# Kernel optimization log

Hardware: AMD Instinct MI355X
Metric: run time of the kernel (lower is better)

## Reference

```python
import jax, jax.numpy as jnp
import numpy as np

BATCH, N_STEPS, STATE_DIM = 8192, 128, 16
HIDDEN = 50
IN0 = STATE_DIM + 1  # features + prev_delta


def _lstm_cell(x, h, c, w_ih, w_hh, b):
    # PyTorch gate order: i, f, g, o
    gates = x @ w_ih.T + h @ w_hh.T + b  # (B, 4H)
    i, f, g, o = jnp.split(gates, 4, axis=-1)
    c_new = jax.nn.sigmoid(f) * c + jax.nn.sigmoid(i) * jnp.tanh(g)
    h_new = jax.nn.sigmoid(o) * jnp.tanh(c_new)
    return h_new, c_new


def setup_inputs() -> dict:
    key = jax.random.key(0)
    ks = jax.random.split(key, 8)
    s = 0.1
    return {
        "features": jax.random.normal(ks[0], (BATCH, N_STEPS, STATE_DIM), dtype=jnp.float32),
        "w_ih0": jax.random.normal(ks[1], (4 * HIDDEN, IN0), dtype=jnp.float32) * s,
        "w_hh0": jax.random.normal(ks[2], (4 * HIDDEN, HIDDEN), dtype=jnp.float32) * s,
        "b_0": jnp.zeros((4 * HIDDEN,), dtype=jnp.float32),  # bias_ih + bias_hh (both init to 0)
        "w_ih1": jax.random.normal(ks[3], (4 * HIDDEN, HIDDEN), dtype=jnp.float32) * s,
        "w_hh1": jax.random.normal(ks[4], (4 * HIDDEN, HIDDEN), dtype=jnp.float32) * s,
        "b_1": jnp.zeros((4 * HIDDEN,), dtype=jnp.float32),
        "w_fc1": jax.random.normal(ks[5], (HIDDEN // 2, HIDDEN), dtype=jnp.float32) * s,
        "b_fc1": jnp.zeros((HIDDEN // 2,), dtype=jnp.float32),
        "w_fc2": jax.random.normal(ks[6], (1, HIDDEN // 2), dtype=jnp.float32) * s,
        "b_fc2": jnp.zeros((1,), dtype=jnp.float32),
    }


def reference(features, w_ih0, w_hh0, b_0, w_ih1, w_hh1, b_1, w_fc1, b_fc1, w_fc2, b_fc2):
    B = features.shape[0]
    feats_t = jnp.swapaxes(features, 0, 1)  # (T, B, state_dim)
    z = jnp.zeros((B, HIDDEN), dtype=features.dtype)
    init = (z, z, z, z, jnp.zeros((B, 1), dtype=features.dtype))

    def step(carry, x_t):
        h0, c0, h1, c1, prev_delta = carry
        x = jnp.concatenate([x_t, prev_delta], axis=-1)  # (B, state_dim+1)
        h0, c0 = _lstm_cell(x, h0, c0, w_ih0, w_hh0, b_0)
        h1, c1 = _lstm_cell(h0, h1, c1, w_ih1, w_hh1, b_1)
        delta = jax.nn.relu(h1 @ w_fc1.T + b_fc1) @ w_fc2.T + b_fc2  # (B, 1)
        return (h0, c0, h1, c1, delta), delta[:, 0]

    _, deltas = jax.lax.scan(step, init, feats_t)  # (T, B)
    return jnp.swapaxes(deltas, 0, 1)  # (B, T)
```

## Files before the change

kernel.cpp:

```cpp
#include <hip/hip_runtime.h>
#include <math.h>

#define BATCH    8192
#define TSTEPS   128
#define SDIM     16
#define HID      50
#define IN0      17
#define BT       16
#define NTHREADS 512

#define RS      168
#define OFF_H0  32
#define OFF_H1  96
#define W0K     96
#define W1K     128
#define WFK     64

typedef _Float16 half_t;
typedef __attribute__((ext_vector_type(8))) _Float16 half8;
typedef __attribute__((ext_vector_type(4))) float    floatx4;

#define MFMA16(a, b, c) __builtin_amdgcn_mfma_f32_16x16x32_f16((a), (b), (c), 0, 0, 0)

__device__ __forceinline__ float sig_u(float x) {
    float e = __expf(-x);
    return __builtin_amdgcn_rcpf(1.0f + e);
}
__device__ __forceinline__ float tanh_u(float x) {
    float e = __expf(-2.0f * x);
    return fmaf(2.0f, __builtin_amdgcn_rcpf(1.0f + e), -1.0f);
}
__device__ __forceinline__ void hsplit(float v, half_t* hp, half_t* lp) {
    half_t h = (half_t)v;
    *hp = h;
    *lp = (half_t)(v - (float)h);
}

__global__ __launch_bounds__(NTHREADS, 4)
void lstm2_w8_kernel(const float* __restrict__ feat,
                     const float* __restrict__ w_ih0,
                     const float* __restrict__ w_hh0,
                     const float* __restrict__ b_0,
                     const float* __restrict__ w_ih1,
                     const float* __restrict__ w_hh1,
                     const float* __restrict__ b_1,
                     const float* __restrict__ w_fc1,
                     const float* __restrict__ b_fc1,
                     const float* __restrict__ w_fc2,
                     const float* __restrict__ b_fc2,
                     float* __restrict__ out)
{
    __shared__ __align__(16) half_t smW[64 * W1K];
    __shared__ __align__(16) half_t Xh[2][BT * RS];
    __shared__ __align__(16) half_t Xl[2][BT * RS];

    const int tid  = threadIdx.x;
    const int lane = tid & 63;
    const int wv   = tid >> 6;
    const int quad = lane >> 4;
    const int col  = lane & 15;
    const int k0q  = quad * 8;
    const int b0   = blockIdx.x * BT;
    const int tcnt = (wv < 6) ? 2 : (wv == 6 ? 1 : 0);

    auto w0val = [&](int r, int k) -> float {
        if (r >= 200) return 0.0f;
        int j = r >> 2, q = r & 3, orig = q * HID + j;
        if (k < IN0)  return w_ih0[orig * IN0 + k];
        if (k == IN0) return b_0[orig];
        if (k < OFF_H0) return 0.0f;
        int u = k - OFF_H0;
        return (u < HID) ? w_hh0[orig * HID + u] : 0.0f;
    };
    auto w1val = [&](int r, int k) -> float {
        if (r >= 200) return 0.0f;
        int j = r >> 2, q = r & 3, orig = q * HID + j;
        if (k < 64) {
            if (k < HID)  return w_ih1[orig * HID + k];
            if (k == HID) return b_1[orig];
            return 0.0f;
        }
        int u = k - 64;
        return (u < HID) ? w_hh1[orig * HID + u] : 0.0f;
    };

    half8 a0f[3][2], a1f[4][2];
    const int lbase = 32 * (wv & 1) + col;
    #pragma unroll 1
    for (int c = 0; c < 4; ++c) {
        for (int i = tid; i < 64 * W0K; i += NTHREADS) {
            int r = i / W0K, k = i - r * W0K;
            smW[i] = (half_t)w0val(64 * c + r, k);
        }
        __syncthreads();
        if ((wv >> 1) == c) {
            #pragma unroll
            for (int kt = 0; kt < 3; ++kt)
                #pragma unroll
                for (int ti = 0; ti < 2; ++ti)
                    a0f[kt][ti] = *(const half8*)(smW + (lbase + 16 * ti) * W0K + 32 * kt + k0q);
        }
        __syncthreads();
    }
    #pragma unroll 1
    for (int c = 0; c < 4; ++c) {
        for (int i = tid; i < 64 * W1K; i += NTHREADS) {
            int r = i >> 7, k = i & 127;
            smW[i] = (half_t)w1val(64 * c + r, k);
        }
        __syncthreads();
        if ((wv >> 1) == c) {
            #pragma unroll
            for (int kt = 0; kt < 4; ++kt)
                #pragma unroll
                for (int ti = 0; ti < 2; ++ti)
                    a1f[kt][ti] = *(const half8*)(smW + (lbase + 16 * ti) * W1K + 32 * kt + k0q);
        }
        __syncthreads();
    }
    for (int i = tid; i < 32 * WFK; i += NTHREADS) {
        int r = i >> 6, k = i & 63;
        float v = 0.0f;
        if (r < 25) { if (k < HID) v = w_fc1[r * HID + k]; else if (k == HID) v = b_fc1[r]; }
        smW[i] = (half_t)v;
    }
    __syncthreads();
    half8 wff[2][2];
    #pragma unroll
    for (int kt = 0; kt < 2; ++kt)
        #pragma unroll
        for (int tf = 0; tf < 2; ++tf)
            wff[kt][tf] = *(const half8*)(smW + (16 * tf + col) * WFK + 32 * kt + k0q);

    for (int i = tid; i < BT * RS; i += NTHREADS) {
        Xh[0][i] = (half_t)0.0f; Xl[0][i] = (half_t)0.0f;
        Xh[1][i] = (half_t)0.0f; Xl[1][i] = (half_t)0.0f;
    }
    __syncthreads();
    if (tid < BT) {
        Xh[0][tid * RS + OFF_H0 + HID] = (half_t)1.0f;
        Xh[1][tid * RS + OFF_H0 + HID] = (half_t)1.0f;
        Xh[0][tid * RS + OFF_H1 + HID] = (half_t)1.0f;
        Xh[1][tid * RS + OFF_H1 + HID] = (half_t)1.0f;
    }
    const bool stager = (tid < BT * SDIM);
    const int  xs = tid >> 4, xk = tid & 15;
    const size_t fbase = (size_t)(b0 + (stager ? xs : 0)) * (TSTEPS * SDIM) + xk;
    if (stager) hsplit(feat[fbase], &Xh[0][xs * RS + xk], &Xl[0][xs * RS + xk]);

    floatx4 w2r[2];
    { floatx4 z = {0.f, 0.f, 0.f, 0.f}; w2r[0] = z; w2r[1] = z; }
    #pragma unroll
    for (int tf = 0; tf < 2; ++tf)
        #pragma unroll
        for (int r5 = 0; r5 < 4; ++r5) {
            int r = 16 * tf + 4 * quad + r5;
            if (r < 25) w2r[tf][r5] = w_fc2[r];
        }
    const float bf2 = b_fc2[0];

    const half8   hz = {0, 0, 0, 0, 0, 0, 0, 0};
    const floatx4 fz = {0.f, 0.f, 0.f, 0.f};
    float c0s[2] = {0.f, 0.f};
    float c1s[2] = {0.f, 0.f};
    half_t dh = (half_t)0.0f, dl = (half_t)0.0f;

    half_t* Xhc = Xh[0]; half_t* Xlc = Xl[0];
    half_t* Xhn = Xh[1]; half_t* Xln = Xl[1];
    __syncthreads();

    for (int t = 0; t < TSTEPS; ++t) {
        float fnext = 0.0f;
        if (stager && (t + 1 < TSTEPS)) fnext = feat[fbase + (size_t)(t + 1) * SDIM];

        floatx4 acc[2]; acc[0] = fz; acc[1] = fz;
        if (tcnt > 0) {
            half8 bh0, bl0;
            if (quad < 2) {
                bh0 = *(const half8*)(Xhc + col * RS + k0q);
                bl0 = *(const half8*)(Xlc + col * RS + k0q);
            } else {
                bh0 = hz; bl0 = hz;
                if (quad == 2) { bh0[0] = dh; bh0[1] = (half_t)1.0f; bl0[0] = dl; }
            }
            #pragma unroll
            for (int ti = 0; ti < 2; ++ti)
                if (ti < tcnt) {
                    acc[ti] = MFMA16(a0f[0][ti], bh0, acc[ti]);
                    acc[ti] = MFMA16(a0f[0][ti], bl0, acc[ti]);
                }
            #pragma unroll
            for (int kt = 1; kt < 3; ++kt) {
                half8 bh = *(const half8*)(Xhc + col * RS + OFF_H0 + 32 * (kt - 1) + k0q);
                half8 bl = *(const half8*)(Xlc + col * RS + OFF_H0 + 32 * (kt - 1) + k0q);
                #pragma unroll
                for (int ti = 0; ti < 2; ++ti)
                    if (ti < tcnt) {
                        acc[ti] = MFMA16(a0f[kt][ti], bh, acc[ti]);
                        acc[ti] = MFMA16(a0f[kt][ti], bl, acc[ti]);
                    }
            }
        }

        #pragma unroll
        for (int ti = 0; ti < 2; ++ti)
            if (ti < tcnt) {
                int u = 8 * wv + 4 * ti + quad;
                float i_ = sig_u(acc[ti][0]);
                float f_ = sig_u(acc[ti][1]);
                float g_ = tanh_u(acc[ti][2]);
                float o_ = sig_u(acc[ti][3]);
                float c  = f_ * c0s[ti] + i_ * g_;
                c0s[ti]  = c;
                float hv = o_ * tanh_u(c);
                if (u < HID) {
                    half_t hh, hl; hsplit(hv, &hh, &hl);
                    Xhn[col * RS + OFF_H0 + u] = hh;
                    Xln[col * RS + OFF_H0 + u] = hl;
                }
            }
        __syncthreads();

        if (stager && (t + 1 < TSTEPS))
            hsplit(fnext, &Xhn[xs * RS + xk], &Xln[xs * RS + xk]);

        floatx4 acc1[2]; acc1[0] = fz; acc1[1] = fz;
        if (tcnt > 0) {
            #pragma unroll
            for (int kt = 0; kt < 2; ++kt) {
                half8 bh = *(const half8*)(Xhn + col * RS + OFF_H0 + 32 * kt + k0q);
                half8 bl = *(const half8*)(Xln + col * RS + OFF_H0 + 32 * kt + k0q);
                #pragma unroll
                for (int ti = 0; ti < 2; ++ti)
                    if (ti < tcnt) {
                        acc1[ti] = MFMA16(a1f[kt][ti], bh, acc1[ti]);
                        acc1[ti] = MFMA16(a1f[kt][ti], bl, acc1[ti]);
                    }
            }
            #pragma unroll
            for (int kt = 2; kt < 4; ++kt) {
                half8 bh = *(const half8*)(Xhc + col * RS + OFF_H1 + 32 * (kt - 2) + k0q);
                half8 bl = *(const half8*)(Xlc + col * RS + OFF_H1 + 32 * (kt - 2) + k0q);
                #pragma unroll
                for (int ti = 0; ti < 2; ++ti)
                    if (ti < tcnt) {
                        acc1[ti] = MFMA16(a1f[kt][ti], bh, acc1[ti]);
                        acc1[ti] = MFMA16(a1f[kt][ti], bl, acc1[ti]);
                    }
            }
        }

        #pragma unroll
        for (int ti = 0; ti < 2; ++ti)
            if (ti < tcnt) {
                int u = 8 * wv + 4 * ti + quad;
                float i_ = sig_u(acc1[ti][0]);
                float f_ = sig_u(acc1[ti][1]);
                float g_ = tanh_u(acc1[ti][2]);
                float o_ = sig_u(acc1[ti][3]);
                float c  = f_ * c1s[ti] + i_ * g_;
                c1s[ti]  = c;
                float hv = o_ * tanh_u(c);
                if (u < HID) {
                    half_t hh, hl; hsplit(hv, &hh, &hl);
                    Xhn[col * RS + OFF_H1 + u] = hh;
                    Xln[col * RS + OFF_H1 + u] = hl;
                }
            }
        __syncthreads();

        floatx4 accf[2]; accf[0] = fz; accf[1] = fz;
        #pragma unroll
        for (int kt = 0; kt < 2; ++kt) {
            half8 bh = *(const half8*)(Xhn + col * RS + OFF_H1 + 32 * kt + k0q);
            half8 bl = *(const half8*)(Xln + col * RS + OFF_H1 + 32 * kt + k0q);
            #pragma unroll
            for (int tf = 0; tf < 2; ++tf) {
                accf[tf] = MFMA16(wff[kt][tf], bh, accf[tf]);
                accf[tf] = MFMA16(wff[kt][tf], bl, accf[tf]);
            }
        }
        float p = 0.0f;
        #pragma unroll
        for (int tf = 0; tf < 2; ++tf)
            #pragma unroll
            for (int r5 = 0; r5 < 4; ++r5)
                p += w2r[tf][r5] * fmaxf(accf[tf][r5], 0.0f);
        p += __shfl_xor(p, 16);
        p += __shfl_xor(p, 32);
        float d = p + bf2;
        if (wv == 0 && lane < 16)
            out[(size_t)(b0 + lane) * TSTEPS + t] = d;
        hsplit(d, &dh, &dl);

        half_t* tp;
        tp = Xhc; Xhc = Xhn; Xhn = tp;
        tp = Xlc; Xlc = Xln; Xln = tp;
    }
}

extern "C" void kernel_launch(void* const* d_in, const int* in_sizes, int n_in,
                              void* d_out, int out_size, void* d_ws, size_t ws_size,
                              hipStream_t stream) {
    const float* feat  = (const float*)d_in[0];
    const float* w_ih0 = (const float*)d_in[1];
    const float* w_hh0 = (const float*)d_in[2];
    const float* b_0   = (const float*)d_in[3];
    const float* w_ih1 = (const float*)d_in[4];
    const float* w_hh1 = (const float*)d_in[5];
    const float* b_1   = (const float*)d_in[6];
    const float* w_fc1 = (const float*)d_in[7];
    const float* b_fc1 = (const float*)d_in[8];
    const float* w_fc2 = (const float*)d_in[9];
    const float* b_fc2 = (const float*)d_in[10];
    float* out = (float*)d_out;

    dim3 grid(BATCH / BT);
    dim3 block(NTHREADS);
    hipLaunchKernelGGL(lstm2_w8_kernel, grid, block, 0, stream,
                       feat, w_ih0, w_hh0, b_0, w_ih1, w_hh1, b_1,
                       w_fc1, b_fc1, w_fc2, b_fc2, out);
}
```

Measured before the change: 473.3 us.

## Fold biases into accumulators, apply prev-delta in fp32, split hi/lo MFMA chains

Biases move out of the weight matrices and become the initial MFMA accumulator values, and the prev_delta input column is applied as an fp32 FMA after the matmul. This removes the bias/one columns from shared memory and drops the idle 8th wave (448 threads). The hi and lo MFMA products now go to separate accumulators, which breaks the serial dependency chain so two chains can interleave, at the cost of extra registers and a vector add per gate.

```diff
diff --git a/kernel.cpp b/kernel.cpp
--- a/kernel.cpp
+++ b/kernel.cpp
@@ -7,7 +7,7 @@
 #define HID      50
 #define IN0      17
 #define BT       16
-#define NTHREADS 512
+#define NTHREADS 448
 
 #define RS      168
 #define OFF_H0  32
@@ -61,13 +61,11 @@
     const int col  = lane & 15;
     const int k0q  = quad * 8;
     const int b0   = blockIdx.x * BT;
-    const int tcnt = (wv < 6) ? 2 : (wv == 6 ? 1 : 0);
 
     auto w0val = [&](int r, int k) -> float {
         if (r >= 200) return 0.0f;
         int j = r >> 2, q = r & 3, orig = q * HID + j;
-        if (k < IN0)  return w_ih0[orig * IN0 + k];
-        if (k == IN0) return b_0[orig];
+        if (k < SDIM)   return w_ih0[orig * IN0 + k];
         if (k < OFF_H0) return 0.0f;
         int u = k - OFF_H0;
         return (u < HID) ? w_hh0[orig * HID + u] : 0.0f;
@@ -75,11 +73,7 @@
     auto w1val = [&](int r, int k) -> float {
         if (r >= 200) return 0.0f;
         int j = r >> 2, q = r & 3, orig = q * HID + j;
-        if (k < 64) {
-            if (k < HID)  return w_ih1[orig * HID + k];
-            if (k == HID) return b_1[orig];
-            return 0.0f;
-        }
+        if (k < 64) return (k < HID) ? w_ih1[orig * HID + k] : 0.0f;
         int u = k - 64;
         return (u < HID) ? w_hh1[orig * HID + u] : 0.0f;
     };
@@ -121,7 +115,7 @@
     for (int i = tid; i < 32 * WFK; i += NTHREADS) {
         int r = i >> 6, k = i & 63;
         float v = 0.0f;
-        if (r < 25) { if (k < HID) v = w_fc1[r * HID + k]; else if (k == HID) v = b_fc1[r]; }
+        if (r < 25 && k < HID) v = w_fc1[r * HID + k];
         smW[i] = (half_t)v;
     }
     __syncthreads();
@@ -132,17 +126,32 @@
         for (int tf = 0; tf < 2; ++tf)
             wff[kt][tf] = *(const half8*)(smW + (16 * tf + col) * WFK + 32 * kt + k0q);
 
+    floatx4 b0v[2], w16v[2], b1v[2];
+    #pragma unroll
+    for (int ti = 0; ti < 2; ++ti) {
+        int u = 8 * wv + 4 * ti + quad;
+        #pragma unroll
+        for (int r = 0; r < 4; ++r) {
+            int orig = r * HID + u;
+            b0v[ti][r]  = (u < HID) ? b_0[orig] : 0.0f;
+            w16v[ti][r] = (u < HID) ? w_ih0[orig * IN0 + SDIM] : 0.0f;
+            b1v[ti][r]  = (u < HID) ? b_1[orig] : 0.0f;
+        }
+    }
+    floatx4 bfv[2];
+    #pragma unroll
+    for (int tf = 0; tf < 2; ++tf)
+        #pragma unroll
+        for (int r5 = 0; r5 < 4; ++r5) {
+            int rfc = 16 * tf + 4 * quad + r5;
+            bfv[tf][r5] = (rfc < 25) ? b_fc1[rfc] : 0.0f;
+        }
+
     for (int i = tid; i < BT * RS; i += NTHREADS) {
         Xh[0][i] = (half_t)0.0f; Xl[0][i] = (half_t)0.0f;
         Xh[1][i] = (half_t)0.0f; Xl[1][i] = (half_t)0.0f;
     }
     __syncthreads();
-    if (tid < BT) {
-        Xh[0][tid * RS + OFF_H0 + HID] = (half_t)1.0f;
-        Xh[1][tid * RS + OFF_H0 + HID] = (half_t)1.0f;
-        Xh[0][tid * RS + OFF_H1 + HID] = (half_t)1.0f;
-        Xh[1][tid * RS + OFF_H1 + HID] = (half_t)1.0f;
-    }
     const bool stager = (tid < BT * SDIM);
     const int  xs = tid >> 4, xk = tid & 15;
     const size_t fbase = (size_t)(b0 + (stager ? xs : 0)) * (TSTEPS * SDIM) + xk;
@@ -163,7 +172,7 @@
     const floatx4 fz = {0.f, 0.f, 0.f, 0.f};
     float c0s[2] = {0.f, 0.f};
     float c1s[2] = {0.f, 0.f};
-    half_t dh = (half_t)0.0f, dl = (half_t)0.0f;
+    float d_prev = 0.0f;
 
     half_t* Xhc = Xh[0]; half_t* Xlc = Xl[0];
     half_t* Xhn = Xh[1]; half_t* Xln = Xl[1];
@@ -173,103 +182,96 @@
         float fnext = 0.0f;
         if (stager && (t + 1 < TSTEPS)) fnext = feat[fbase + (size_t)(t + 1) * SDIM];
 
-        floatx4 acc[2]; acc[0] = fz; acc[1] = fz;
-        if (tcnt > 0) {
+        floatx4 aH[2], aL[2];
+        aH[0] = b0v[0]; aH[1] = b0v[1]; aL[0] = fz; aL[1] = fz;
+        {
             half8 bh0, bl0;
             if (quad < 2) {
                 bh0 = *(const half8*)(Xhc + col * RS + k0q);
                 bl0 = *(const half8*)(Xlc + col * RS + k0q);
-            } else {
-                bh0 = hz; bl0 = hz;
-                if (quad == 2) { bh0[0] = dh; bh0[1] = (half_t)1.0f; bl0[0] = dl; }
-            }
-            #pragma unroll
-            for (int ti = 0; ti < 2; ++ti)
-                if (ti < tcnt) {
-                    acc[ti] = MFMA16(a0f[0][ti], bh0, acc[ti]);
-                    acc[ti] = MFMA16(a0f[0][ti], bl0, acc[ti]);
-                }
+            } else { bh0 = hz; bl0 = hz; }
+            #pragma unroll
+            for (int ti = 0; ti < 2; ++ti) {
+                aH[ti] = MFMA16(a0f[0][ti], bh0, aH[ti]);
+                aL[ti] = MFMA16(a0f[0][ti], bl0, aL[ti]);
+            }
             #pragma unroll
             for (int kt = 1; kt < 3; ++kt) {
                 half8 bh = *(const half8*)(Xhc + col * RS + OFF_H0 + 32 * (kt - 1) + k0q);
                 half8 bl = *(const half8*)(Xlc + col * RS + OFF_H0 + 32 * (kt - 1) + k0q);
                 #pragma unroll
-                for (int ti = 0; ti < 2; ++ti)
-                    if (ti < tcnt) {
-                        acc[ti] = MFMA16(a0f[kt][ti], bh, acc[ti]);
-                        acc[ti] = MFMA16(a0f[kt][ti], bl, acc[ti]);
-                    }
-            }
-        }
-
-        #pragma unroll
-        for (int ti = 0; ti < 2; ++ti)
-            if (ti < tcnt) {
-                int u = 8 * wv + 4 * ti + quad;
-                float i_ = sig_u(acc[ti][0]);
-                float f_ = sig_u(acc[ti][1]);
-                float g_ = tanh_u(acc[ti][2]);
-                float o_ = sig_u(acc[ti][3]);
-                float c  = f_ * c0s[ti] + i_ * g_;
-                c0s[ti]  = c;
-                float hv = o_ * tanh_u(c);
-                if (u < HID) {
-                    half_t hh, hl; hsplit(hv, &hh, &hl);
-                    Xhn[col * RS + OFF_H0 + u] = hh;
-                    Xln[col * RS + OFF_H0 + u] = hl;
+                for (int ti = 0; ti < 2; ++ti) {
+                    aH[ti] = MFMA16(a0f[kt][ti], bh, aH[ti]);
+                    aL[ti] = MFMA16(a0f[kt][ti], bl, aL[ti]);
                 }
             }
+        }
+
+        #pragma unroll
+        for (int ti = 0; ti < 2; ++ti) {
+            floatx4 g = aH[ti] + aL[ti];
+            int u = 8 * wv + 4 * ti + quad;
+            float i_ = sig_u (g[0] + w16v[ti][0] * d_prev);
+            float f_ = sig_u (g[1] + w16v[ti][1] * d_prev);
+            float g_ = tanh_u(g[2] + w16v[ti][2] * d_prev);
+            float o_ = sig_u (g[3] + w16v[ti][3] * d_prev);
+            float c  = f_ * c0s[ti] + i_ * g_;
+            c0s[ti]  = c;
+            float hv = o_ * tanh_u(c);
+            if (u < HID) {
+                half_t hh, hl; hsplit(hv, &hh, &hl);
+                Xhn[col * RS + OFF_H0 + u] = hh;
+                Xln[col * RS + OFF_H0 + u] = hl;
+            }
+        }
         __syncthreads();
 
         if (stager && (t + 1 < TSTEPS))
             hsplit(fnext, &Xhn[xs * RS + xk], &Xln[xs * RS + xk]);
 
-        floatx4 acc1[2]; acc1[0] = fz; acc1[1] = fz;
-        if (tcnt > 0) {
-            #pragma unroll
-            for (int kt = 0; kt < 2; ++kt) {
-                half8 bh = *(const half8*)(Xhn + col * RS + OFF_H0 + 32 * kt + k0q);
-                half8 bl = *(const half8*)(Xln + col * RS + OFF_H0 + 32 * kt + k0q);
-                #pragma unroll
-                for (int ti = 0; ti < 2; ++ti)
-                    if (ti < tcnt) {
-                        acc1[ti] = MFMA16(a1f[kt][ti], bh, acc1[ti]);
-                        acc1[ti] = MFMA16(a1f[kt][ti], bl, acc1[ti]);
-                    }
-            }
-            #pragma unroll
-            for (int kt = 2; kt < 4; ++kt) {
-                half8 bh = *(const half8*)(Xhc + col * RS + OFF_H1 + 32 * (kt - 2) + k0q);
-                half8 bl = *(const half8*)(Xlc + col * RS + OFF_H1 + 32 * (kt - 2) + k0q);
-                #pragma unroll
-                for (int ti = 0; ti < 2; ++ti)
-                    if (ti < tcnt) {
-                        acc1[ti] = MFMA16(a1f[kt][ti], bh, acc1[ti]);
-                        acc1[ti] = MFMA16(a1f[kt][ti], bl, acc1[ti]);
-                    }
-            }
-        }
-
-        #pragma unroll
-        for (int ti = 0; ti < 2; ++ti)
-            if (ti < tcnt) {
-                int u = 8 * wv + 4 * ti + quad;
-                float i_ = sig_u(acc1[ti][0]);
-                float f_ = sig_u(acc1[ti][1]);
-                float g_ = tanh_u(acc1[ti][2]);
-                float o_ = sig_u(acc1[ti][3]);
-                float c  = f_ * c1s[ti] + i_ * g_;
-                c1s[ti]  = c;
-                float hv = o_ * tanh_u(c);
-                if (u < HID) {
-                    half_t hh, hl; hsplit(hv, &hh, &hl);
-                    Xhn[col * RS + OFF_H1 + u] = hh;
-                    Xln[col * RS + OFF_H1 + u] = hl;
-                }
-            }
-        __syncthreads();
-
-        floatx4 accf[2]; accf[0] = fz; accf[1] = fz;
+        floatx4 a1H[2], a1L[2];
+        a1H[0] = b1v[0]; a1H[1] = b1v[1]; a1L[0] = fz; a1L[1] = fz;
+        #pragma unroll
+        for (int kt = 0; kt < 2; ++kt) {
+            half8 bh = *(const half8*)(Xhn + col * RS + OFF_H0 + 32 * kt + k0q);
+            half8 bl = *(const half8*)(Xln + col * RS + OFF_H0 + 32 * kt + k0q);
+            #pragma unroll
+            for (int ti = 0; ti < 2; ++ti) {
+                a1H[ti] = MFMA16(a1f[kt][ti], bh, a1H[ti]);
+                a1L[ti] = MFMA16(a1f[kt][ti], bl, a1L[ti]);
+            }
+        }
+        #pragma unroll
+        for (int kt = 2; kt < 4; ++kt) {
+            half8 bh = *(const half8*)(Xhc + col * RS + OFF_H1 + 32 * (kt - 2) + k0q);
+            half8 bl = *(const half8*)(Xlc + col * RS + OFF_H1 + 32 * (kt - 2) + k0q);
+            #pragma unroll
+            for (int ti = 0; ti < 2; ++ti) {
+                a1H[ti] = MFMA16(a1f[kt][ti], bh, a1H[ti]);
+                a1L[ti] = MFMA16(a1f[kt][ti], bl, a1L[ti]);
+            }
+        }
+
+        #pragma unroll
+        for (int ti = 0; ti < 2; ++ti) {
+            floatx4 g = a1H[ti] + a1L[ti];
+            int u = 8 * wv + 4 * ti + quad;
+            float i_ = sig_u (g[0]);
+            float f_ = sig_u (g[1]);
+            float g_ = tanh_u(g[2]);
+            float o_ = sig_u (g[3]);
+            float c  = f_ * c1s[ti] + i_ * g_;
+            c1s[ti]  = c;
+            float hv = o_ * tanh_u(c);
+            if (u < HID) {
+                half_t hh, hl; hsplit(hv, &hh, &hl);
+                Xhn[col * RS + OFF_H1 + u] = hh;
+                Xln[col * RS + OFF_H1 + u] = hl;
+            }
+        }
+        __syncthreads();
+
+        floatx4 accf[2]; accf[0] = bfv[0]; accf[1] = bfv[1];
         #pragma unroll
         for (int kt = 0; kt < 2; ++kt) {
             half8 bh = *(const half8*)(Xhn + col * RS + OFF_H1 + 32 * kt + k0q);
@@ -291,7 +293,7 @@
         float d = p + bf2;
         if (wv == 0 && lane < 16)
             out[(size_t)(b0 + lane) * TSTEPS + t] = d;
-        hsplit(d, &dh, &dl);
+        d_prev = d;
 
         half_t* tp;
         tp = Xhc; Xhc = Xhn; Xhn = tp;
```

New measurement: 1.262 ms. +166.6%, slower.
